# Kernel tuning notes

Hardware: AMD Instinct MI355X
Metric: run time of the kernel (lower is better)

The kernel has to match this reference:

```python
import jax, jax.numpy as jnp
import numpy as np

BETA, THR, ALPHA = 0.9, 1.0, 2.0  # snn.Leaky defaults from neuron_options + surrogate.atan(alpha=2)

# Heaviside spike with atan surrogate gradient (snntorch surrogate.atan)
@jax.custom_vjp
def spike(u):
    return (u > 0).astype(u.dtype)

def _spk_fwd(u):
    return (u > 0).astype(u.dtype), u

def _spk_bwd(u, g):
    return ((ALPHA / 2) / (1 + (jnp.pi / 2 * ALPHA * u) ** 2) * g,)

spike.defvjp(_spk_fwd, _spk_bwd)


def setup_inputs() -> dict:
    key = jax.random.key(0)
    ks = jax.random.split(key, 4)
    B, T, I, H1, H2, O = 128, 128, 1024, 2048, 2048, 512
    return {
        "x": jax.random.normal(ks[0], (B, T, I), jnp.float32),
        "W1": jax.random.normal(ks[1], (H1, I), jnp.float32) * 0.02,
        "b1": jnp.zeros((H1,), jnp.float32),
        "W2": jax.random.normal(ks[2], (H2, H1), jnp.float32) * 0.02,
        "b2": jnp.zeros((H2,), jnp.float32),
        "Wout": jax.random.normal(ks[3], (O, H2), jnp.float32) * 0.02,
        "bout": jnp.zeros((O,), jnp.float32),
    }


def _lif(v_prev, cur):
    # Module calls snn.Leaky as spike_layer(in_volt, x) -> forward(input_=v_prev, mem=cur).
    # snntorch Leaky ('subtract' reset): reset = H(mem - thr) [detached];
    # mem_new = beta*mem + input_ - reset*thr; spk = H(mem_new - thr) with atan surrogate.
    reset = jax.lax.stop_gradient((cur > THR).astype(cur.dtype))
    mem = BETA * cur + v_prev - reset * THR
    return spike(mem - THR), mem


def reference(x, W1, b1, W2, b2, Wout, bout):
    B, T, I = x.shape
    H1, H2 = W1.shape[0], W2.shape[0]
    v0 = (jnp.zeros((B, H1), x.dtype), jnp.zeros((B, H2), x.dtype))

    def step(vs, x_t):
        v1, v2 = vs
        s1, v1n = _lif(v1, x_t @ W1.T + b1)   # linear -> LIF layer 1
        s2, v2n = _lif(v2, s1 @ W2.T + b2)    # linear -> LIF layer 2
        return (v1n, v2n), s2

    _, spikes = jax.lax.scan(step, v0, jnp.swapaxes(x, 0, 1))  # spikes: (T, B, H2)
    acc = spikes.mean(0)  # 'sum' accumulator = mean over time of last-layer spikes
    return acc @ Wout.T + bout  # fc_out, identity activation
```

## Files before the change

kernel.cpp:

```cpp
#include <hip/hip_runtime.h>


typedef unsigned long long u64;
typedef __attribute__((ext_vector_type(4))) float f32x4;
typedef __attribute__((ext_vector_type(8))) short bf16x8;
typedef __attribute__((ext_vector_type(4))) int i32x4;

__device__ __forceinline__ unsigned short f2bf(float f) {
  unsigned u = __float_as_uint(f);
  u += 0x7fff + ((u >> 16) & 1);
  return (unsigned short)(u >> 16);
}
__device__ __forceinline__ float bf2f(unsigned short h) {
  return __uint_as_float(((unsigned)h) << 16);
}
__device__ __forceinline__ void gld_lds16(const void* g, void* l) {
  __builtin_amdgcn_global_load_lds((const __attribute__((address_space(1))) void*)g,
                                   (__attribute__((address_space(3))) void*)l, 16, 0, 0);
}

__global__ void k_split4(const float4* __restrict__ src, unsigned short* __restrict__ dst,
                         int lgK, size_t total4) {
  size_t i = (size_t)blockIdx.x * 256 + threadIdx.x;
  if (i >= total4) return;
  const int K = 1 << lgK;
  size_t e = i << 2;
  size_t r = e >> lgK;
  int k = (int)(e & (size_t)(K - 1));
  float4 f = src[i];
  unsigned short h0 = f2bf(f.x), h1 = f2bf(f.y), h2 = f2bf(f.z), h3 = f2bf(f.w);
  unsigned short l0 = f2bf(f.x - bf2f(h0)), l1 = f2bf(f.y - bf2f(h1));
  unsigned short l2 = f2bf(f.z - bf2f(h2)), l3 = f2bf(f.w - bf2f(h3));
  size_t o = (r << (lgK + 1)) + (size_t)k;
  *(u64*)(dst + o)     = (u64)h0 | ((u64)h1 << 16) | ((u64)h2 << 32) | ((u64)h3 << 48);
  *(u64*)(dst + o + K) = (u64)l0 | ((u64)l1 << 16) | ((u64)l2 << 32) | ((u64)l3 << 48);
}

__global__ void k_quant_w2(const float* __restrict__ W2, signed char* __restrict__ W2q,
                           float* __restrict__ scl) {
  __shared__ float red[4];
  const int r = blockIdx.x;
  const int tid = threadIdx.x;
  const float* row = W2 + (size_t)r * 2048;
  float vbuf[8];
  float mx = 0.f;
#pragma unroll
  for (int k = 0; k < 8; ++k) {
    vbuf[k] = row[tid + k * 256];
    mx = fmaxf(mx, fabsf(vbuf[k]));
  }
#pragma unroll
  for (int o = 32; o; o >>= 1) mx = fmaxf(mx, __shfl_xor(mx, o));
  if ((tid & 63) == 0) red[tid >> 6] = mx;
  __syncthreads();
  mx = fmaxf(fmaxf(red[0], red[1]), fmaxf(red[2], red[3]));
  mx = fmaxf(mx, 1e-20f);
  const float inv = 127.f / mx;
  if (tid == 0) scl[r] = mx * (1.f / 127.f);
#pragma unroll
  for (int k = 0; k < 8; ++k)
    W2q[(size_t)r * 2048 + tid + k * 256] = (signed char)__float2int_rn(vbuf[k] * inv);
}

#define DSR4(D, BASE)                                                          \
  do {                                                                         \
    asm volatile("ds_read_b128 %0, %1" : "=v"(D[0]) : "v"(BASE));              \
    asm volatile("ds_read_b128 %0, %1 offset:2048" : "=v"(D[1]) : "v"(BASE));  \
    asm volatile("ds_read_b128 %0, %1 offset:4096" : "=v"(D[2]) : "v"(BASE));  \
    asm volatile("ds_read_b128 %0, %1 offset:6144" : "=v"(D[3]) : "v"(BASE));  \
  } while (0)
#define DSR4_I8(D, BASE)                                                       \
  do {                                                                         \
    asm volatile("ds_read_b128 %0, %1" : "=v"(D[0]) : "v"(BASE));              \
    asm volatile("ds_read_b128 %0, %1 offset:1024" : "=v"(D[1]) : "v"(BASE));  \
    asm volatile("ds_read_b128 %0, %1 offset:2048" : "=v"(D[2]) : "v"(BASE));  \
    asm volatile("ds_read_b128 %0, %1 offset:3072" : "=v"(D[3]) : "v"(BASE));  \
  } while (0)
#define WAITL(N)                                                               \
  do {                                                                         \
    asm volatile("s_waitcnt lgkmcnt(" #N ")" ::: "memory");                    \
    __builtin_amdgcn_sched_barrier(0);                                         \
  } while (0)
#define VMC(N)                                                                 \
  do {                                                                         \
    asm volatile("s_waitcnt vmcnt(" #N ")" ::: "memory");                      \
    __builtin_amdgcn_sched_barrier(0);                                         \
  } while (0)
#define BAR() __builtin_amdgcn_s_barrier()
#define SP1() __builtin_amdgcn_s_setprio(1)
#define SP0() __builtin_amdgcn_s_setprio(0)
#define MFMA16(MH, AF, BG)                                                     \
  _Pragma("unroll")                                                            \
  for (int m = 0; m < 4; ++m)                                                  \
    _Pragma("unroll")                                                          \
    for (int n = 0; n < 4; ++n)                                                \
      acc[(MH)*4 + m][n] = __builtin_amdgcn_mfma_f32_16x16x32_bf16(            \
          AF[m], BG[n], acc[(MH)*4 + m][n], 0, 0, 0);
#define MFMA16_I8(MH, AF, BG)                                                  \
  _Pragma("unroll")                                                            \
  for (int m = 0; m < 4; ++m)                                                  \
    _Pragma("unroll")                                                          \
    for (int n = 0; n < 4; ++n)                                                \
      acc[(MH)*4 + m][n] = __builtin_amdgcn_mfma_i32_16x16x64_i8(              \
          AF[m], BG[n], acc[(MH)*4 + m][n], 0, 0, 0);

__global__ __launch_bounds__(512, 2)
void k_gemm1_lif(const unsigned short* __restrict__ A,
                 const unsigned short* __restrict__ Bw,
                 const float* __restrict__ bias,
                 unsigned char* __restrict__ out) {
  __shared__ __align__(128) char lds[132096];
  const int NKT = 48;
  const int tid  = threadIdx.x;
  const int lane = tid & 63;
  const int w    = tid >> 6;
  const int wm = w >> 2, wn = w & 3;
  const int wr = wm * 128, wc = wn * 64;
  const int lrow = lane & 15, t4 = lane >> 4;
  const int brow = blockIdx.x * 256, bcol = blockIdx.y * 256;

  f32x4 acc[8][4];
#pragma unroll
  for (int m = 0; m < 8; ++m)
#pragma unroll
    for (int n = 0; n < 4; ++n) acc[m][n] = (f32x4){0.f, 0.f, 0.f, 0.f};

  int voffA[4], voffB[4];
  unsigned dstA[4], dstB[4];
#pragma unroll
  for (int j = 0; j < 4; ++j) {
    const int c = tid + j * 512;
    const int r = c >> 3;
    const int scol = ((c & 7) ^ (r & 7)) * 8;
    voffA[j] = (brow + r) * 2048 + scol;
    voffB[j] = (bcol + r) * 2048 + scol;
    dstA[j] = (unsigned)c * 16;
    dstB[j] = 32768u + (unsigned)c * 16;
  }
  auto stage_tile = [&](int tt) {
    if (tt >= NKT) return;
    const int kb = tt * 64;
    const int aoff = (kb < 1024) ? kb : kb - 1024;
    const int boff = (kb < 2048) ? kb : kb - 2048;
    const unsigned short* Ap = A + aoff;
    const unsigned short* Bp = Bw + boff;
    char* slot = lds + (tt & 1) * 65536;
#pragma unroll
    for (int j = 0; j < 4; ++j)
      gld_lds16(Ap + voffA[j], slot + dstA[j]);
#pragma unroll
    for (int j = 0; j < 4; ++j)
      gld_lds16(Bp + voffB[j], slot + dstB[j]);
  };

  const unsigned ldsb = (unsigned)(size_t)(__attribute__((address_space(3))) char*)lds;
  const unsigned cA   = (unsigned)((wr + lrow) * 128);
  const unsigned cB   = (unsigned)(32768 + (wc + lrow) * 128);
  const unsigned ch0  = (unsigned)(((t4) ^ (lrow & 7)) * 16);
  const unsigned ch1  = (unsigned)(((4 + t4) ^ (lrow & 7)) * 16);

  bf16x8 afA[4], afB[4], bgA[4], bgB[4];

  stage_tile(0);
  asm volatile("s_waitcnt vmcnt(0)" ::: "memory");
  BAR();
  DSR4(afA, ldsb + cA + ch0);
  DSR4(bgA, ldsb + cB + ch0);

#pragma unroll 1
  for (int t = 0; t < NKT; ++t) {
    const unsigned sA  = ldsb + (unsigned)((t & 1) * 65536);
    const unsigned sAn = ldsb + (unsigned)(((t + 1) & 1) * 65536);
    stage_tile(t + 1);
    DSR4(afB, sA + cA + 8192 + ch0);
    WAITL(4);
    SP1(); MFMA16(0, afA, bgA); SP0();
    DSR4(afA, sA + cA + ch1);
    DSR4(bgB, sA + cB + ch1);
    WAITL(8);
    SP1(); MFMA16(1, afB, bgA); SP0();
    DSR4(afB, sA + cA + 8192 + ch1);
    WAITL(4);
    SP1(); MFMA16(0, afA, bgB); SP0();
    asm volatile("s_waitcnt vmcnt(0)" ::: "memory");
    BAR();
    if (t + 1 < NKT) {
      DSR4(afA, sAn + cA + ch0);
      DSR4(bgA, sAn + cB + ch0);
      WAITL(8);
    } else {
      WAITL(0);
    }
    SP1(); MFMA16(1, afB, bgB); SP0();
    BAR();
  }

  float* Ct = (float*)lds;
  const int colT  = tid & 255;
  const int batch = tid >> 8;
  const float bs = bias[bcol + colT];
  float v = 0.f;
  unsigned char* sp = out + (size_t)(brow + batch * 128) * 2048 + bcol + colT;
#pragma unroll
  for (int h = 0; h < 2; ++h) {
    __syncthreads();
#pragma unroll
    for (int mm = 0; mm < 4; ++mm) {
      const int m = h * 4 + mm;
#pragma unroll
      for (int n = 0; n < 4; ++n) {
        const int lr  = wm * 64 + mm * 16 + t4 * 4;
        const int col = wc + n * 16 + lrow;
#pragma unroll
        for (int r = 0; r < 4; ++r) Ct[(lr + r) * 258 + col] = acc[m][n][r];
      }
    }
    __syncthreads();
#pragma unroll 4
    for (int tl = 0; tl < 64; ++tl) {
      const float xx = Ct[(batch * 64 + tl) * 258 + colT] + bs;
      v = 0.9f * xx + v - ((xx > 1.0f) ? 1.0f : 0.0f);
      sp[(size_t)(h * 64 + tl) * 2048] = (v > 1.0f) ? 1 : 0;
    }
  }
}

__global__ __launch_bounds__(512, 2)
void k_gemm2_lif_i8(const signed char* __restrict__ A,
                    const signed char* __restrict__ Bq,
                    const float* __restrict__ scl,
                    const float* __restrict__ bias,
                    unsigned short* __restrict__ out, int b0) {
  __shared__ __align__(128) char lds[132096];
  const int NKT = 32;
  const int tid  = threadIdx.x;
  const int lane = tid & 63;
  const int w    = tid >> 6;
  const int wm = w >> 2, wn = w & 3;
  const int wr = wm * 128, wc = wn * 64;
  const int lrow = lane & 15, t4 = lane >> 4;
  const int brow = blockIdx.x * 256, bcol = blockIdx.y * 256;

  i32x4 acc[8][4];
#pragma unroll
  for (int m = 0; m < 8; ++m)
#pragma unroll
    for (int n = 0; n < 4; ++n) acc[m][n] = (i32x4){0, 0, 0, 0};

  int voffA[2], voffB[2];
  unsigned dstA[2], dstB[2];
#pragma unroll
  for (int j = 0; j < 2; ++j) {
    const int c = tid + j * 512;
    const int r = c >> 2;
    const int sc = ((c & 3) ^ ((r >> 1) & 3)) * 16;
    voffA[j] = (brow + r) * 2048 + sc;
    voffB[j] = (bcol + r) * 2048 + sc;
    dstA[j] = (unsigned)c * 16;
    dstB[j] = 16384u + (unsigned)c * 16;
  }
  auto stage_tile = [&](int tt) {
    if (tt >= NKT) return;
    const int kb = tt * 64;
    char* slot = lds + (tt % 3) * 32768;
#pragma unroll
    for (int j = 0; j < 2; ++j)
      gld_lds16(A + kb + voffA[j], slot + dstA[j]);
#pragma unroll
    for (int j = 0; j < 2; ++j)
      gld_lds16(Bq + kb + voffB[j], slot + dstB[j]);
  };

  const unsigned ldsb = (unsigned)(size_t)(__attribute__((address_space(3))) char*)lds;
  const unsigned cA  = (unsigned)((wr + lrow) * 64);
  const unsigned cB  = 16384u + (unsigned)((wc + lrow) * 64);
  const unsigned chi = (unsigned)((t4 ^ ((lrow >> 1) & 3)) * 16);

  i32x4 afA[4], afB[4], bgA[4], bgB[4];

  stage_tile(0); stage_tile(1);
  VMC(4);
  BAR();
  DSR4_I8(afA, ldsb + cA + chi);
  DSR4_I8(bgA, ldsb + cB + chi);

#define TILE_I8(T, BGC, BGN)                                                   \
  {                                                                            \
    const int tt = (T);                                                        \
    const unsigned s  = ldsb + (unsigned)((tt % 3) * 32768);                   \
    const unsigned sn = ldsb + (unsigned)(((tt + 1) % 3) * 32768);             \
    stage_tile(tt + 2);                                                        \
    if (tt + 2 < NKT) { VMC(4); } else { VMC(0); }       \
    BAR();                                                                     \
    DSR4_I8(afB, s + cA + 4096 + chi);                                         \
    WAITL(4);                                                                  \
    SP1(); MFMA16_I8(0, afA, BGC); SP0();                                      \
    if (tt + 1 < NKT) {                                                        \
      DSR4_I8(afA, sn + cA + chi);                                             \
      DSR4_I8(BGN, sn + cB + chi);                                             \
      WAITL(8);                                                                \
    } else {                                                                   \
      WAITL(0);                                                                \
    }                                                                          \
    SP1(); MFMA16_I8(1, afB, BGC); SP0();                                      \
    BAR();                                                                     \
  }

#pragma unroll 1
  for (int t = 0; t < NKT; t += 2) {
    TILE_I8(t, bgA, bgB);
    TILE_I8(t + 1, bgB, bgA);
  }
#undef TILE_I8

  int* Cti = (int*)lds;
  const int colT  = tid & 255;
  const int batch = tid >> 8;
  const float bs = bias[bcol + colT];
  const float sc = scl[bcol + colT];
  float v = 0.f;
  int cnt = 0;
#pragma unroll
  for (int h = 0; h < 2; ++h) {
    __syncthreads();
#pragma unroll
    for (int mm = 0; mm < 4; ++mm) {
      const int m = h * 4 + mm;
#pragma unroll
      for (int n = 0; n < 4; ++n) {
        const int lr  = wm * 64 + mm * 16 + t4 * 4;
        const int col = wc + n * 16 + lrow;
#pragma unroll
        for (int r = 0; r < 4; ++r) Cti[(lr + r) * 258 + col] = acc[m][n][r];
      }
    }
    __syncthreads();
#pragma unroll 4
    for (int tl = 0; tl < 64; ++tl) {
      const float xx = (float)Cti[(batch * 64 + tl) * 258 + colT] * sc + bs;
      v = 0.9f * xx + v - ((xx > 1.0f) ? 1.0f : 0.0f);
      cnt += (v > 1.0f);
    }
  }
  out[(size_t)(b0 + 2 * blockIdx.x + batch) * 2048 + bcol + colT] =
      f2bf((float)cnt * 0.0078125f);
}

__global__ void k_gemm3(const unsigned short* __restrict__ A,
                        const unsigned short* __restrict__ B,
                        float* __restrict__ C) {
  __shared__ __align__(16) unsigned short Asm[128 * 64];
  __shared__ __align__(16) unsigned short Bsm[128 * 64];
  const int tid  = threadIdx.x;
  const int bcol = blockIdx.y * 128;
  const int k0   = blockIdx.z * 256;
  const int lane = tid & 63;
  const int w    = tid >> 6;
  const int wr = (w >> 1) * 64, wc = (w & 1) * 64;
  const int lrow = lane & 15, lk = (lane >> 4) * 8;

  f32x4 acc[4][4];
#pragma unroll
  for (int m = 0; m < 4; ++m)
#pragma unroll
    for (int n = 0; n < 4; ++n) acc[m][n] = (f32x4){0.f, 0.f, 0.f, 0.f};

  for (int kt = 0; kt < 4; ++kt) {
    const int kb = k0 + kt * 64;
#pragma unroll
    for (int i = 0; i < 4; ++i) {
      int c = tid + i * 256;
      int row = c >> 3, kc = (c & 7) * 8;
      gld_lds16(A + (size_t)row * 2048 + (kb & 2047) + kc, &Asm[c * 8]);
      gld_lds16(B + (size_t)(bcol + row) * 4096 + kb + kc, &Bsm[c * 8]);
    }
    __syncthreads();
#pragma unroll
    for (int ks = 0; ks < 2; ++ks) {
      bf16x8 af[4], bg[4];
#pragma unroll
      for (int m = 0; m < 4; ++m)
        af[m] = *(const bf16x8*)&Asm[(wr + m * 16 + lrow) * 64 + ks * 32 + lk];
#pragma unroll
      for (int n = 0; n < 4; ++n)
        bg[n] = *(const bf16x8*)&Bsm[(wc + n * 16 + lrow) * 64 + ks * 32 + lk];
#pragma unroll
      for (int m = 0; m < 4; ++m)
#pragma unroll
        for (int n = 0; n < 4; ++n)
          acc[m][n] = __builtin_amdgcn_mfma_f32_16x16x32_bf16(af[m], bg[n], acc[m][n], 0, 0, 0);
    }
    __syncthreads();
  }
#pragma unroll
  for (int m = 0; m < 4; ++m)
#pragma unroll
    for (int n = 0; n < 4; ++n) {
      int r0 = wr + m * 16 + (lane >> 4) * 4;
      int c0 = bcol + wc + n * 16 + (lane & 15);
#pragma unroll
      for (int r = 0; r < 4; ++r)
        atomicAdd(&C[(size_t)(r0 + r) * 512 + c0], acc[m][n][r]);
    }
}

__global__ void k_init_out(float* __restrict__ out, const float* __restrict__ bout) {
  int i = blockIdx.x * 256 + threadIdx.x;
  out[i] = bout[i & 511];
}

extern "C" void kernel_launch(void* const* d_in, const int* in_sizes, int n_in,
                              void* d_out, int out_size, void* d_ws, size_t ws_size,
                              hipStream_t stream) {
  const float* x    = (const float*)d_in[0];
  const float* W1   = (const float*)d_in[1];
  const float* b1   = (const float*)d_in[2];
  const float* W2   = (const float*)d_in[3];
  const float* b2   = (const float*)d_in[4];
  const float* Wout = (const float*)d_in[5];
  const float* bout = (const float*)d_in[6];
  float* out = (float*)d_out;
  (void)in_sizes; (void)n_in; (void)out_size;

  char* ws = (char*)d_ws;
  size_t off = 0;
  auto alloc = [&](size_t bytes) -> void* {
    void* p = ws + off;
    off += (bytes + 255) & ~(size_t)255;
    return p;
  };
  unsigned short* W1cat = (unsigned short*)alloc((size_t)2048 * 2048 * 2);
  signed char*    W2q   = (signed char*)alloc((size_t)2048 * 2048);
  float*          scl   = (float*)alloc((size_t)2048 * 4);
  unsigned short* Wocat = (unsigned short*)alloc((size_t)512 * 4096 * 2);
  unsigned short* ACC   = (unsigned short*)alloc((size_t)128 * 2048 * 2);
  const size_t fixed = off;

  int rows_c = 16384;
  while (rows_c > 1024) {
    size_t per = (((size_t)rows_c * 2048 * 2 + 255) & ~(size_t)255) +
                 (((size_t)rows_c * 2048 + 255) & ~(size_t)255);
    if (fixed + per <= ws_size) break;
    rows_c >>= 1;
  }
  unsigned short* Xcat = (unsigned short*)alloc((size_t)rows_c * 2048 * 2);
  unsigned char*  S1c  = (unsigned char*)alloc((size_t)rows_c * 2048);

  k_split4<<<(2048 * 256 + 255) / 256, 256, 0, stream>>>((const float4*)W1, W1cat, 10,
                                                         (size_t)2048 * 256);
  k_quant_w2<<<2048, 256, 0, stream>>>(W2, W2q, scl);
  k_split4<<<(512 * 512 + 255) / 256, 256, 0, stream>>>((const float4*)Wout, Wocat, 11,
                                                        (size_t)512 * 512);

  const int nch = 16384 / rows_c;
  for (int c = 0; c < nch; ++c) {
    k_split4<<<rows_c, 256, 0, stream>>>((const float4*)(x + (size_t)c * rows_c * 1024),
                                         Xcat, 10, (size_t)rows_c * 256);
    k_gemm1_lif<<<dim3(rows_c / 256, 8), 512, 0, stream>>>(Xcat, W1cat, b1, S1c);
    k_gemm2_lif_i8<<<dim3(rows_c / 256, 8), 512, 0, stream>>>(
        (const signed char*)S1c, W2q, scl, b2, ACC, c * (rows_c / 128));
  }
  k_init_out<<<256, 256, 0, stream>>>(out, bout);
  k_gemm3<<<dim3(1, 4, 16), 256, 0, stream>>>(ACC, Wocat, out);
}
```

Baseline: 283.9 us.

## Restructure bf16 GEMM1 pipeline to triple-buffered 32-wide K tiles

The bf16 GEMM1+LIF kernel now uses K tiles of 32 instead of 64, with three LDS buffers of 32 KB in place of two of 64 KB. Loads run two tiles ahead, matching the existing int8 GEMM2 pipeline, and the XOR swizzle is adapted to 64-byte rows. The aim is to hide global-load latency behind MFMA work with a deeper prefetch and a lighter per-tile vmcnt wait. In exchange the kernel runs twice as many iterations, each with two barriers, and smaller tiles per sync.

```diff
diff --git a/kernel.cpp b/kernel.cpp
--- a/kernel.cpp
+++ b/kernel.cpp
@@ -62,14 +62,7 @@
     W2q[(size_t)r * 2048 + tid + k * 256] = (signed char)__float2int_rn(vbuf[k] * inv);
 }
 
-#define DSR4(D, BASE)                                                          \
-  do {                                                                         \
-    asm volatile("ds_read_b128 %0, %1" : "=v"(D[0]) : "v"(BASE));              \
-    asm volatile("ds_read_b128 %0, %1 offset:2048" : "=v"(D[1]) : "v"(BASE));  \
-    asm volatile("ds_read_b128 %0, %1 offset:4096" : "=v"(D[2]) : "v"(BASE));  \
-    asm volatile("ds_read_b128 %0, %1 offset:6144" : "=v"(D[3]) : "v"(BASE));  \
-  } while (0)
-#define DSR4_I8(D, BASE)                                                       \
+#define DSR4_64(D, BASE)                                                       \
   do {                                                                         \
     asm volatile("ds_read_b128 %0, %1" : "=v"(D[0]) : "v"(BASE));              \
     asm volatile("ds_read_b128 %0, %1 offset:1024" : "=v"(D[1]) : "v"(BASE));  \
@@ -110,7 +103,7 @@
                  const float* __restrict__ bias,
                  unsigned char* __restrict__ out) {
   __shared__ __align__(128) char lds[132096];
-  const int NKT = 48;
+  const int NKT = 96;
   const int tid  = threadIdx.x;
   const int lane = tid & 63;
   const int w    = tid >> 6;
@@ -125,75 +118,75 @@
 #pragma unroll
     for (int n = 0; n < 4; ++n) acc[m][n] = (f32x4){0.f, 0.f, 0.f, 0.f};
 
-  int voffA[4], voffB[4];
-  unsigned dstA[4], dstB[4];
-#pragma unroll
-  for (int j = 0; j < 4; ++j) {
+  int voffA[2], voffB[2];
+  unsigned dstA[2], dstB[2];
+#pragma unroll
+  for (int j = 0; j < 2; ++j) {
     const int c = tid + j * 512;
-    const int r = c >> 3;
-    const int scol = ((c & 7) ^ (r & 7)) * 8;
-    voffA[j] = (brow + r) * 2048 + scol;
-    voffB[j] = (bcol + r) * 2048 + scol;
+    const int r = c >> 2;
+    const int sc = ((c & 3) ^ ((r >> 1) & 3)) * 8;
+    voffA[j] = (brow + r) * 2048 + sc;
+    voffB[j] = (bcol + r) * 2048 + sc;
     dstA[j] = (unsigned)c * 16;
-    dstB[j] = 32768u + (unsigned)c * 16;
+    dstB[j] = 16384u + (unsigned)c * 16;
   }
   auto stage_tile = [&](int tt) {
     if (tt >= NKT) return;
-    const int kb = tt * 64;
+    const int kb = tt * 32;
     const int aoff = (kb < 1024) ? kb : kb - 1024;
     const int boff = (kb < 2048) ? kb : kb - 2048;
     const unsigned short* Ap = A + aoff;
     const unsigned short* Bp = Bw + boff;
-    char* slot = lds + (tt & 1) * 65536;
-#pragma unroll
-    for (int j = 0; j < 4; ++j)
+    char* slot = lds + (tt % 3) * 32768;
+#pragma unroll
+    for (int j = 0; j < 2; ++j)
       gld_lds16(Ap + voffA[j], slot + dstA[j]);
 #pragma unroll
-    for (int j = 0; j < 4; ++j)
+    for (int j = 0; j < 2; ++j)
       gld_lds16(Bp + voffB[j], slot + dstB[j]);
   };
 
   const unsigned ldsb = (unsigned)(size_t)(__attribute__((address_space(3))) char*)lds;
-  const unsigned cA   = (unsigned)((wr + lrow) * 128);
-  const unsigned cB   = (unsigned)(32768 + (wc + lrow) * 128);
-  const unsigned ch0  = (unsigned)(((t4) ^ (lrow & 7)) * 16);
-  const unsigned ch1  = (unsigned)(((4 + t4) ^ (lrow & 7)) * 16);
+  const unsigned cA  = (unsigned)((wr + lrow) * 64);
+  const unsigned cB  = 16384u + (unsigned)((wc + lrow) * 64);
+  const unsigned chi = (unsigned)((t4 ^ ((lrow >> 1) & 3)) * 16);
 
   bf16x8 afA[4], afB[4], bgA[4], bgB[4];
 
-  stage_tile(0);
-  asm volatile("s_waitcnt vmcnt(0)" ::: "memory");
+  stage_tile(0); stage_tile(1);
+  VMC(4);
   BAR();
-  DSR4(afA, ldsb + cA + ch0);
-  DSR4(bgA, ldsb + cB + ch0);
+  DSR4_64(afA, ldsb + cA + chi);
+  DSR4_64(bgA, ldsb + cB + chi);
+
+#define TILE_B32(T, BGC, BGN)                                                  \
+  {                                                                            \
+    const int tt = (T);                                                        \
+    const unsigned s  = ldsb + (unsigned)((tt % 3) * 32768);                   \
+    const unsigned sn = ldsb + (unsigned)(((tt + 1) % 3) * 32768);             \
+    stage_tile(tt + 2);                                                        \
+    if (tt + 2 < NKT) { VMC(4); } else { VMC(0); }       \
+    BAR();                                                                     \
+    DSR4_64(afB, s + cA + 4096 + chi);                                         \
+    WAITL(4);                                                                  \
+    SP1(); MFMA16(0, afA, BGC); SP0();                                         \
+    if (tt + 1 < NKT) {                                                        \
+      DSR4_64(afA, sn + cA + chi);                                             \
+      DSR4_64(BGN, sn + cB + chi);                                             \
+      WAITL(8);                                                                \
+    } else {                                                                   \
+      WAITL(0);                                                                \
+    }                                                                          \
+    SP1(); MFMA16(1, afB, BGC); SP0();                                         \
+    BAR();                                                                     \
+  }
 
 #pragma unroll 1
-  for (int t = 0; t < NKT; ++t) {
-    const unsigned sA  = ldsb + (unsigned)((t & 1) * 65536);
-    const unsigned sAn = ldsb + (unsigned)(((t + 1) & 1) * 65536);
-    stage_tile(t + 1);
-    DSR4(afB, sA + cA + 8192 + ch0);
-    WAITL(4);
-    SP1(); MFMA16(0, afA, bgA); SP0();
-    DSR4(afA, sA + cA + ch1);
-    DSR4(bgB, sA + cB + ch1);
-    WAITL(8);
-    SP1(); MFMA16(1, afB, bgA); SP0();
-    DSR4(afB, sA + cA + 8192 + ch1);
-    WAITL(4);
-    SP1(); MFMA16(0, afA, bgB); SP0();
-    asm volatile("s_waitcnt vmcnt(0)" ::: "memory");
-    BAR();
-    if (t + 1 < NKT) {
-      DSR4(afA, sAn + cA + ch0);
-      DSR4(bgA, sAn + cB + ch0);
-      WAITL(8);
-    } else {
-      WAITL(0);
-    }
-    SP1(); MFMA16(1, afB, bgB); SP0();
-    BAR();
-  }
+  for (int t = 0; t < NKT; t += 2) {
+    TILE_B32(t, bgA, bgB);
+    TILE_B32(t + 1, bgB, bgA);
+  }
+#undef TILE_B32
 
   float* Ct = (float*)lds;
   const int colT  = tid & 255;
@@ -281,8 +274,8 @@
   stage_tile(0); stage_tile(1);
   VMC(4);
   BAR();
-  DSR4_I8(afA, ldsb + cA + chi);
-  DSR4_I8(bgA, ldsb + cB + chi);
+  DSR4_64(afA, ldsb + cA + chi);
+  DSR4_64(bgA, ldsb + cB + chi);
 
 #define TILE_I8(T, BGC, BGN)                                                   \
   {                                                                            \
@@ -290,14 +283,14 @@
     const unsigned s  = ldsb + (unsigned)((tt % 3) * 32768);                   \
     const unsigned sn = ldsb + (unsigned)(((tt + 1) % 3) * 32768);             \
     stage_tile(tt + 2);                                                        \
-    if (tt + 2 < NKT) { VMC(4); } else { VMC(0); }       \
+    if (tt + 2 < NKT) { VMC(4); } else { VMC(0); }                             \
     BAR();                                                                     \
-    DSR4_I8(afB, s + cA + 4096 + chi);                                         \
+    DSR4_64(afB, s + cA + 4096 + chi);                                         \
     WAITL(4);                                                                  \
     SP1(); MFMA16_I8(0, afA, BGC); SP0();                                      \
     if (tt + 1 < NKT) {                                                        \
-      DSR4_I8(afA, sn + cA + chi);                                             \
-      DSR4_I8(BGN, sn + cB + chi);                                             \
+      DSR4_64(afA, sn + cA + chi);                                             \
+      DSR4_64(BGN, sn + cB + chi);                                             \
       WAITL(8);                                                                \
     } else {                                                                   \
       WAITL(0);                                                                \
```

New measurement: 297.6 us. 4.8% more time.
